# Kernel optimization log

Hardware: AMD Instinct MI355X
Metric: run time of the kernel (lower is better)

## Reference

```python
import jax, jax.numpy as jnp
import numpy as np

E, K, CAP = 6, 2, 192
ALPHA, LOAD_PEN, MIN_USE, TEMP = 0.7, 2.0, 0.05, 1.0
BN_EPS = 1e-5
NEG = -1e30


def conv3x3(x, w, b=None):
    y = jax.lax.conv_general_dilated(x, w, (1, 1), 'SAME',
                                     dimension_numbers=('NCHW', 'OIHW', 'NCHW'))
    if b is not None:
        y = y + b[None, :, None, None]
    return y


def bn_eval(x, g, b):
    # fresh BatchNorm buffers: running_mean=0, running_var=1
    s = g / jnp.sqrt(1.0 + BN_EPS)
    return x * s[None, :, None, None] + b[None, :, None, None]


def maxpool2(x):
    return jax.lax.reduce_window(x, -jnp.inf, jax.lax.max,
                                 (1, 1, 2, 2), (1, 1, 2, 2), 'VALID')


def avgpool_to2(x):
    B, C, H, W = x.shape
    return x.reshape(B, C, 2, H // 2, 2, W // 2).mean(axis=(3, 5))


def expert_forward(p, x):
    h = jax.nn.relu(bn_eval(conv3x3(x, p['c1w'], p['c1b']), p['b1g'], p['b1b']))
    h = maxpool2(h)  # 32 -> 16
    h = jax.nn.relu(bn_eval(conv3x3(h, p['c2w'], p['c2b']), p['b2g'], p['b2b']))
    h = jax.nn.relu(bn_eval(conv3x3(h, p['c3w'], p['c3b']), p['b3g'], p['b3b']))
    h = maxpool2(h)  # 16 -> 8
    h = jax.nn.relu(bn_eval(conv3x3(h, p['c4w'], p['c4b']), p['b4g'], p['b4b']))
    h = jax.nn.relu(bn_eval(conv3x3(h, p['c5w'], p['c5b']), p['b5g'], p['b5b']))
    feat = h.mean(axis=(2, 3))                       # global avg pool -> [B, c3]
    f = jax.nn.relu(feat @ p['fw'].T + p['fb'])      # [B, feat_dim]
    return f @ p['cw'].T + p['cb']                   # [B, num_classes]


def moe_forward(x, t_c1w, t_b1g, t_b1b, t_c2w, t_b2g, t_b2b, t_fcw, t_fcb,
                g1w, g1b, g2w, g2b,
                e_c1w, e_c1b, e_b1g, e_b1b, e_c2w, e_c2b, e_b2g, e_b2b,
                e_c3w, e_c3b, e_b3g, e_b3b, e_c4w, e_c4b, e_b4g, e_b4b,
                e_c5w, e_c5b, e_b5g, e_b5b, e_fw, e_fb, e_cw, e_cb, ema):
    B = x.shape[0]
    # --- routing trunk ---
    h = jax.nn.relu(bn_eval(conv3x3(x, t_c1w), t_b1g, t_b1b))
    h = jax.nn.relu(bn_eval(conv3x3(h, t_c2w), t_b2g, t_b2b))
    h = avgpool_to2(maxpool2(h)).reshape(B, -1)      # [B, 128]
    rf = jax.nn.relu(h @ t_fcw.T + t_fcb)            # [B, routing_dim]
    # --- gate (eval: no dropout, no noise) ---
    g = jax.nn.relu(rf @ g1w.T + g1b)
    gate_scores = (g @ g2w.T + g2b) / TEMP           # [B, E]
    # --- all experts on full batch (dense, as in source) ---
    ep = {'c1w': e_c1w, 'c1b': e_c1b, 'b1g': e_b1g, 'b1b': e_b1b,
          'c2w': e_c2w, 'c2b': e_c2b, 'b2g': e_b2g, 'b2b': e_b2b,
          'c3w': e_c3w, 'c3b': e_c3b, 'b3g': e_b3g, 'b3b': e_b3b,
          'c4w': e_c4w, 'c4b': e_c4b, 'b4g': e_b4g, 'b4b': e_b4b,
          'c5w': e_c5w, 'c5b': e_c5b, 'b5g': e_b5g, 'b5b': e_b5b,
          'fw': e_fw, 'fb': e_fb, 'cw': e_cw, 'cb': e_cb}
    logits_e = jax.vmap(expert_forward, in_axes=(0, None))(ep, x)  # [E, B, C]
    logits_e = jnp.transpose(logits_e, (1, 0, 2))                   # [B, E, C]
    # confidence = -entropy = sum p*log(p)
    logp = jax.nn.log_softmax(logits_e, axis=2)
    conf = (jnp.exp(logp) * jnp.log(jnp.exp(logp) + 1e-12)).sum(axis=2)  # [B, E]
    # --- balanced scores ---
    combined = ALPHA * gate_scores + (1.0 - ALPHA) * conf
    boost = jnp.where(ema < MIN_USE, (MIN_USE - ema) * 10.0, 0.0)
    combined = combined + boost[None, :]
    balanced = combined - LOAD_PEN * ema[None, :]
    # --- greedy capacity-constrained dispatch (deterministic order, eval) ---
    _, topk_idx = jax.lax.top_k(balanced, K)          # [B, K]

    def step(loads, idxs):
        l = loads[idxs]                                # [K]
        fits = l < CAP
        first = jnp.argmax(fits)                       # first expert with room
        fallback = idxs[jnp.argmin(l)]
        chosen = jnp.where(fits.any(), idxs[first], fallback)
        return loads.at[chosen].add(1.0), chosen

    _, chosen = jax.lax.scan(step, jnp.zeros((E,), balanced.dtype), topk_idx)
    D = jax.nn.one_hot(chosen, E, dtype=bool)          # [B, E]
    # --- weighted combine ---
    masked = jnp.where(D, balanced, NEG)
    w = jax.nn.softmax(masked, axis=1) * D.astype(balanced.dtype)
    w = w / (w.sum(axis=1, keepdims=True) + 1e-12)
    logits_final = (w[:, :, None] * logits_e).sum(axis=1)  # [B, C]
    return logits_final, balanced, D


def _params(key):
    ks = iter(jax.random.split(key, 64))
    rd, rd2, fd, nc, c1, c2, c3 = 64, 32, 128, 10, 32, 64, 128

    def w(shape, fan):
        return jax.random.normal(next(ks), shape, jnp.float32) * np.sqrt(2.0 / fan)

    p = {}
    p['t_c1w'] = w((32, 3, 3, 3), 32 * 9); p['t_b1g'] = jnp.ones(32); p['t_b1b'] = jnp.zeros(32)
    p['t_c2w'] = w((32, 32, 3, 3), 32 * 9); p['t_b2g'] = jnp.ones(32); p['t_b2b'] = jnp.zeros(32)
    p['t_fcw'] = w((rd, 128), rd); p['t_fcb'] = jnp.zeros(rd)
    p['g1w'] = w((rd2, rd), rd2); p['g1b'] = jnp.zeros(rd2)
    p['g2w'] = w((E, rd2), E); p['g2b'] = jnp.zeros(E)
    for i, (ci, co) in enumerate([(3, c1), (c1, c2), (c2, c2), (c2, c3), (c3, c3)], 1):
        p[f'e_c{i}w'] = w((E, co, ci, 3, 3), co * 9)
        p[f'e_c{i}b'] = jnp.zeros((E, co))
        p[f'e_b{i}g'] = jnp.ones((E, co))
        p[f'e_b{i}b'] = jnp.zeros((E, co))
    p['e_fw'] = w((E, fd, c3), fd); p['e_fb'] = jnp.zeros((E, fd))
    p['e_cw'] = w((E, nc, fd), nc); p['e_cb'] = jnp.zeros((E, nc))
    p['ema'] = jnp.ones((E,), jnp.float32) / E
    return p


def setup_inputs() -> dict:
    key = jax.random.key(0)
    kx, kp = jax.random.split(key)
    inp = {'x': jax.random.normal(kx, (1024, 3, 32, 32), jnp.float32)}
    inp.update(_params(kp))
    return inp


def reference(x, t_c1w, t_b1g, t_b1b, t_c2w, t_b2g, t_b2b, t_fcw, t_fcb,
              g1w, g1b, g2w, g2b,
              e_c1w, e_c1b, e_b1g, e_b1b, e_c2w, e_c2b, e_b2g, e_b2b,
              e_c3w, e_c3b, e_b3g, e_b3b, e_c4w, e_c4b, e_b4g, e_b4b,
              e_c5w, e_c5b, e_b5g, e_b5b, e_fw, e_fb, e_cw, e_cb, ema):
    return moe_forward(x, t_c1w, t_b1g, t_b1b, t_c2w, t_b2g, t_b2b, t_fcw, t_fcb,
                       g1w, g1b, g2w, g2b,
                       e_c1w, e_c1b, e_b1g, e_b1b, e_c2w, e_c2b, e_b2g, e_b2b,
                       e_c3w, e_c3b, e_b3g, e_b3b, e_c4w, e_c4b, e_b4g, e_b4b,
                       e_c5w, e_c5b, e_b5g, e_b5b, e_fw, e_fb, e_cw, e_cb, ema)
```

## Files before the change

### kernel.cpp

```cpp
#include <hip/hip_runtime.h>
#include <math.h>

#define B_ 1024
#define E_ 6

typedef _Float16 half8 __attribute__((ext_vector_type(8)));
typedef float f32x4 __attribute__((ext_vector_type(4)));

__device__ __forceinline__ unsigned short h_bits(_Float16 h) {
    union { _Float16 f; unsigned short u; } c; c.f = h; return c.u;
}
__device__ __forceinline__ unsigned int splitpack(float v) {
    _Float16 h = (_Float16)v;
    _Float16 l = (_Float16)((v - (float)h) * 2048.0f);
    return (unsigned int)h_bits(h) | ((unsigned int)h_bits(l) << 16);
}

__global__ void prep_w(const float* __restrict__ w, const float* __restrict__ g,
                       float* __restrict__ wout, int CO, int CI, int total) {
    int i = blockIdx.x * 256 + threadIdx.x;
    if (i >= total) return;
    int k = i % 9;
    int t = i / 9;
    int ci = t % CI; t /= CI;
    int co = t % CO;
    int e  = t / CO;
    float s = g[e * CO + co] * (1.0f / sqrtf(1.0f + 1e-5f));
    wout[(((long)(e * CI + ci) * 9 + k) * CO) + co] = w[i] * s;
}

__global__ void prep_b(const float* __restrict__ cb, const float* __restrict__ g,
                       const float* __restrict__ bb, float* __restrict__ bout, int N) {
    int i = blockIdx.x * 256 + threadIdx.x;
    if (i >= N) return;
    float s = g[i] * (1.0f / sqrtf(1.0f + 1e-5f));
    float c = (cb != nullptr) ? cb[i] : 0.0f;
    bout[i] = c * s + bb[i];
}

__global__ void prep_wfrag(const float* __restrict__ w, const float* __restrict__ g,
                           _Float16* __restrict__ out, int CI, int CO, int total) {
    int i = blockIdx.x * 256 + threadIdx.x;
    if (i >= total) return;
    const int NC = CI / 32;
    const int NB = CO / 16;
    int j = i & 7;
    int lane = (i >> 3) & 63;
    int rest = i >> 9;
    int chunk = rest % NC; rest /= NC;
    int tap = rest % 9; rest /= 9;
    int nbg = rest % NB;
    int e = rest / NB;
    int co = nbg * 16 + (lane & 15);
    int ci = chunk * 32 + ((lane >> 4) * 8) + j;
    float s = g[e * CO + co] * (1.0f / sqrtf(1.0f + 1e-5f));
    float v = w[(((long)(e * CO + co) * CI + ci) * 9) + tap] * s;
    _Float16 hi = (_Float16)v;
    _Float16 lo = (_Float16)((v - (float)hi) * 2048.0f);
    long perE = (long)NB * 9 * NC * 2 * 512;
    long F0 = ((long)(nbg * 9 + tap) * NC + chunk) * 2;
    long base = (long)e * perE + F0 * 512 + lane * 8 + j;
    out[base] = hi;
    out[base + 512] = lo;
}

template <int CI, int CO, int H, int TS, int CO_BLK, int CI_CHUNK, bool POOL, int OUTMODE>
__launch_bounds__(256)
__global__ void conv3x3(const float* __restrict__ in, const float* __restrict__ wt,
                        const float* __restrict__ bias, void* __restrict__ outv) {
    constexpr int TD = H / TS;
    constexpr int TILES = TD * TD;
    constexpr int LW = TS + 2;
    constexpr int NPX = POOL ? (TS / 2) * (TS / 2) : TS * TS;
    constexpr int G = 256 / NPX;
    constexpr int NG = CO / CO_BLK;
    constexpr int GPT = NG / G;
    constexpr int COT = GPT * CO_BLK;
    constexpr int NW = POOL ? 4 : 1;
    constexpr int OD = POOL ? TS / 2 : TS;

    __shared__ float lds[CI_CHUNK * LW * LW];

    int bid = blockIdx.x;
    int n = bid / TILES;
    int t = bid % TILES;
    int ty = (t / TD) * TS;
    int tx = (t % TD) * TS;
    int tid = threadIdx.x;
    int px = tid % NPX;
    int cg0 = tid / NPX;
    const int cg0s = __builtin_amdgcn_readfirstlane(cg0);
    int oy = px / OD;
    int ox = px % OD;

    float acc[NW][COT];
#pragma unroll
    for (int g2 = 0; g2 < GPT; ++g2)
#pragma unroll
        for (int j = 0; j < CO_BLK; ++j) {
            float bv = bias[(cg0s + g2 * G) * CO_BLK + j];
#pragma unroll
            for (int p = 0; p < NW; ++p) acc[p][g2 * CO_BLK + j] = bv;
        }

    for (int cc = 0; cc < CI / CI_CHUNK; ++cc) {
        const float* inb = in + ((long)n * CI + cc * CI_CHUNK) * (H * H);
        for (int idx = tid; idx < CI_CHUNK * LW * LW; idx += 256) {
            int ci = idx / (LW * LW);
            int r = idx - ci * (LW * LW);
            int yy = r / LW + ty - 1;
            int xx = r % LW + tx - 1;
            float v = 0.0f;
            if ((unsigned)yy < (unsigned)H && (unsigned)xx < (unsigned)H)
                v = inb[ci * H * H + yy * H + xx];
            lds[idx] = v;
        }
        __syncthreads();

        const float* wbase = wt + ((long)cc * CI_CHUNK) * 9 * CO;
        for (int ci = 0; ci < CI_CHUNK; ++ci) {
#pragma unroll
            for (int ky = 0; ky < 3; ++ky) {
#pragma unroll
                for (int kx = 0; kx < 3; ++kx) {
                    float v[NW];
                    if constexpr (POOL) {
#pragma unroll
                        for (int dy = 0; dy < 2; ++dy)
#pragma unroll
                            for (int dx = 0; dx < 2; ++dx)
                                v[dy * 2 + dx] =
                                    lds[ci * LW * LW + (2 * oy + dy + ky) * LW + (2 * ox + dx + kx)];
                    } else {
                        v[0] = lds[ci * LW * LW + (oy + ky) * LW + (ox + kx)];
                    }
                    const float* wr = wbase + ((ci * 3 + ky) * 3 + kx) * CO + cg0s * CO_BLK;
#pragma unroll
                    for (int g2 = 0; g2 < GPT; ++g2)
#pragma unroll
                        for (int j = 0; j < CO_BLK; ++j) {
                            float wv = wr[g2 * G * CO_BLK + j];
#pragma unroll
                            for (int p = 0; p < NW; ++p)
                                acc[p][g2 * CO_BLK + j] = fmaf(v[p], wv, acc[p][g2 * CO_BLK + j]);
                        }
                }
            }
        }
        __syncthreads();
    }

    if constexpr (OUTMODE == 1) {
        unsigned int* po = (unsigned int*)outv;
        long base;
        if constexpr (POOL) {
            constexpr int HP = H / 2;
            int pp = (ty / 2 + oy) * HP + (tx / 2 + ox);
            base = ((long)n * (HP * HP) + pp) * CO;
        } else {
            int pp = (ty + oy) * H + (tx + ox);
            base = ((long)n * (H * H) + pp) * CO;
        }
#pragma unroll
        for (int g2 = 0; g2 < GPT; ++g2) {
            int cobase = (cg0s + g2 * G) * CO_BLK;
#pragma unroll
            for (int j4 = 0; j4 < CO_BLK; j4 += 4) {
                uint4 u;
                unsigned int* up = (unsigned int*)&u;
#pragma unroll
                for (int jj = 0; jj < 4; ++jj) {
                    int a = g2 * CO_BLK + j4 + jj;
                    float v;
                    if constexpr (POOL)
                        v = fmaxf(fmaxf(acc[0][a], acc[1][a]), fmaxf(acc[2][a], acc[3][a]));
                    else
                        v = acc[0][a];
                    up[jj] = splitpack(fmaxf(v, 0.0f));
                }
                *(uint4*)(po + base + cobase + j4) = u;
            }
        }
    } else {
        float* out = (float*)outv;
        if constexpr (POOL) {
            constexpr int HP = H / 2;
            int py = ty / 2 + oy;
            int pxx = tx / 2 + ox;
#pragma unroll
            for (int g2 = 0; g2 < GPT; ++g2)
#pragma unroll
                for (int j = 0; j < CO_BLK; ++j) {
                    int co = (cg0s + g2 * G) * CO_BLK + j;
                    int a = g2 * CO_BLK + j;
                    float m = fmaxf(fmaxf(acc[0][a], acc[1][a]), fmaxf(acc[2][a], acc[3][a]));
                    out[((long)n * CO + co) * (HP * HP) + py * HP + pxx] = fmaxf(m, 0.0f);
                }
        } else {
            int yy = ty + oy;
            int xx = tx + ox;
#pragma unroll
            for (int g2 = 0; g2 < GPT; ++g2)
#pragma unroll
                for (int j = 0; j < CO_BLK; ++j) {
                    int co = (cg0s + g2 * G) * CO_BLK + j;
                    out[((long)n * CO + co) * (H * H) + yy * H + xx] =
                        fmaxf(acc[0][g2 * CO_BLK + j], 0.0f);
                }
        }
    }
}

__launch_bounds__(256, 2)
__global__ void conv_mfma_t2(const unsigned int* __restrict__ in,
                             const _Float16* __restrict__ wt,
                             const float* __restrict__ bias,
                             float* __restrict__ rf, int n0) {
    constexpr int PXS = 40;
    __shared__ _Float16 ldsH[18 * 18 * PXS];
    __shared__ _Float16 ldsL[18 * 18 * PXS];
    __shared__ float red[4][32];

    const int tid = threadIdx.x;
    const int wv = tid >> 6, lane = tid & 63;
    const int q = lane >> 4, l15 = lane & 15;
    const int bid = blockIdx.x;
    const int nl = bid >> 2, tile = bid & 3;
    const int ty2 = (tile >> 1) * 16, tx2 = (tile & 1) * 16;

    f32x4 accH[8], accL[8];
#pragma unroll
    for (int i = 0; i < 8; ++i) { accH[i] = (f32x4){0,0,0,0}; accL[i] = (f32x4){0,0,0,0}; }

    for (int u = tid; u < 18 * 18 * 8; u += 256) {
        int cu = u & 7;
        int p = u >> 3;
        int wy = p / 18, wx = p % 18;
        int gy = ty2 + wy - 1, gx = tx2 + wx - 1;
        uint4 w = make_uint4(0, 0, 0, 0);
        if ((unsigned)gy < 32u && (unsigned)gx < 32u)
            w = *(const uint4*)(in + ((long)nl * 1024 + gy * 32 + gx) * 32 + cu * 4);
        unsigned int h01 = (w.x & 0xffffu) | (w.y << 16);
        unsigned int h23 = (w.z & 0xffffu) | (w.w << 16);
        unsigned int l01 = (w.x >> 16) | (w.y & 0xffff0000u);
        unsigned int l23 = (w.z >> 16) | (w.w & 0xffff0000u);
        int fi = (wy * 18 + wx) * PXS + cu * 4;
        *(uint2*)(&ldsH[fi]) = make_uint2(h01, h23);
        *(uint2*)(&ldsL[fi]) = make_uint2(l01, l23);
    }
    __syncthreads();

#pragma unroll
    for (int ky = 0; ky < 3; ++ky)
#pragma unroll
        for (int kx = 0; kx < 3; ++kx) {
            const int tap = ky * 3 + kx;
            half8 ah[4], al[4];
#pragma unroll
            for (int mb = 0; mb < 4; ++mb) {
                int y = wv * 4 + mb;
                int fi = ((y + ky) * 18 + (l15 + kx)) * PXS + q * 8;
                ah[mb] = *(const half8*)&ldsH[fi];
                al[mb] = *(const half8*)&ldsL[fi];
            }
            half8 bh[2], bl[2];
#pragma unroll
            for (int nb = 0; nb < 2; ++nb) {
                int F0 = (nb * 9 + tap) * 2;
                bh[nb] = ((const half8*)wt)[(long)F0 * 64 + lane];
                bl[nb] = ((const half8*)wt)[(long)(F0 + 1) * 64 + lane];
            }
#pragma unroll
            for (int nb = 0; nb < 2; ++nb)
#pragma unroll
                for (int mb = 0; mb < 4; ++mb)
                    accH[mb * 2 + nb] = __builtin_amdgcn_mfma_f32_16x16x32_f16(
                        ah[mb], bh[nb], accH[mb * 2 + nb], 0, 0, 0);
#pragma unroll
            for (int nb = 0; nb < 2; ++nb)
#pragma unroll
                for (int mb = 0; mb < 4; ++mb)
                    accL[mb * 2 + nb] = __builtin_amdgcn_mfma_f32_16x16x32_f16(
                        ah[mb], bl[nb], accL[mb * 2 + nb], 0, 0, 0);
#pragma unroll
            for (int nb = 0; nb < 2; ++nb)
#pragma unroll
                for (int mb = 0; mb < 4; ++mb)
                    accL[mb * 2 + nb] = __builtin_amdgcn_mfma_f32_16x16x32_f16(
                        al[mb], bh[nb], accL[mb * 2 + nb], 0, 0, 0);
        }

    const float inv2048 = 1.0f / 2048.0f;
    float bv[2];
#pragma unroll
    for (int nb = 0; nb < 2; ++nb) bv[nb] = bias[nb * 16 + l15];
    float avg[2] = {0.0f, 0.0f};
#pragma unroll
    for (int k = 0; k < 2; ++k)
#pragma unroll
        for (int j = 0; j < 2; ++j)
#pragma unroll
            for (int nb = 0; nb < 2; ++nb) {
                float m = -1e30f;
#pragma unroll
                for (int dm = 0; dm < 2; ++dm)
#pragma unroll
                    for (int dr = 0; dr < 2; ++dr) {
                        int a = (2 * k + dm) * 2 + nb;
                        int r = 2 * j + dr;
                        float v = accH[a][r] + accL[a][r] * inv2048 + bv[nb];
                        m = fmaxf(m, v);
                    }
                avg[nb] += fmaxf(m, 0.0f);
            }
#pragma unroll
    for (int nb = 0; nb < 2; ++nb) {
        avg[nb] += __shfl_xor(avg[nb], 16);
        avg[nb] += __shfl_xor(avg[nb], 32);
    }
    if (q == 0) {
        red[wv][l15] = avg[0];
        red[wv][16 + l15] = avg[1];
    }
    __syncthreads();
    if (tid < 32) {
        float s = red[0][tid] + red[1][tid] + red[2][tid] + red[3][tid];
        int n = n0 + nl;
        rf[(long)n * 128 + tid * 4 + (tile >> 1) * 2 + (tile & 1)] = s * (1.0f / 64.0f);
    }
}

__launch_bounds__(512, 2)
__global__ void conv_expert(const float* __restrict__ x,
                            const float* __restrict__ w1b, const float* __restrict__ b1b_,
                            const _Float16* __restrict__ wt2b, const float* __restrict__ b2b_,
                            const _Float16* __restrict__ wt3b, const float* __restrict__ b3b_,
                            const _Float16* __restrict__ wt4b, const float* __restrict__ b4b_,
                            const _Float16* __restrict__ wt5b, const float* __restrict__ b5b_,
                            float* __restrict__ featb) {
    __shared__ _Float16 pool[77760];
    _Float16* c2H = pool;
    _Float16* c2L = pool + 12960;
    _Float16* BH  = pool;
    _Float16* BL  = pool + 8000;
    float* xs  = (float*)(pool + 25920);
    float* w1s = (float*)(pool + 25920 + 6936);
    float* b1s = (float*)(pool + 25920 + 6936 + 1728);
    _Float16* AH = pool + 25920;
    _Float16* AL = pool + 51840;
    _Float16* CH = pool + 25920;
    _Float16* CL = pool + 41920;

    const int tid = threadIdx.x;
    const int wv = tid >> 6, lane = tid & 63;
    const int q = lane >> 4, l15 = lane & 15;
    const int rg = wv >> 1, ch2 = wv & 1;
    const int e = blockIdx.x >> 10;
    const int n = blockIdx.x & 1023;
    const float inv2048 = 1.0f / 2048.0f;

    const float* w1 = w1b + e * 864;
    const float* b1 = b1b_ + e * 32;
    const _Float16* wt2 = wt2b + (size_t)e * 36864;
    const float* b2 = b2b_ + e * 64;
    const _Float16* wt3 = wt3b + (size_t)e * 73728;
    const float* b3 = b3b_ + e * 64;
    const _Float16* wt4 = wt4b + (size_t)e * 147456;
    const float* b4 = b4b_ + e * 128;
    const _Float16* wt5 = wt5b + (size_t)e * 294912;
    const float* b5 = b5b_ + e * 128;
    float* feat = featb + (size_t)e * (B_ * 128);

    {
        half8 z = {};
        half8* zp = (half8*)pool;
        for (int i = tid; i < 3240; i += 512) zp[i] = z;
    }
    for (int i = tid; i < 864; i += 512) w1s[i] = w1[i];
    if (tid < 32) b1s[tid] = b1[tid];
    for (int i = tid; i < 3 * 1156; i += 512) {
        int c = i / 1156;
        int r = i - c * 1156;
        int yy = r / 34 - 1, xx = r % 34 - 1;
        float v = 0.0f;
        if ((unsigned)yy < 32u && (unsigned)xx < 32u)
            v = x[((long)n * 3 + c) * 1024 + yy * 32 + xx];
        xs[i] = v;
    }
    __syncthreads();

    {
        const int pix = tid & 255;
        const int py1 = pix >> 4, px1 = pix & 15;
        const int coh = tid >> 8;
#pragma unroll
        for (int cg = 0; cg < 2; ++cg) {
            const int cog = coh * 2 + cg;
            float a[4][8];
#pragma unroll
            for (int j = 0; j < 8; ++j) {
                float bvv = b1s[cog * 8 + j];
#pragma unroll
                for (int p = 0; p < 4; ++p) a[p][j] = bvv;
            }
            for (int ci = 0; ci < 3; ++ci) {
                float patch[16];
#pragma unroll
                for (int r = 0; r < 4; ++r)
#pragma unroll
                    for (int cpx = 0; cpx < 4; ++cpx)
                        patch[r * 4 + cpx] = xs[ci * 1156 + (2 * py1 + r) * 34 + (2 * px1 + cpx)];
#pragma unroll
                for (int ky = 0; ky < 3; ++ky)
#pragma unroll
                    for (int kx = 0; kx < 3; ++kx) {
                        const float* wr = &w1s[((ci * 3 + ky) * 3 + kx) * 32 + cog * 8];
#pragma unroll
                        for (int j = 0; j < 8; ++j) {
                            float wvv = wr[j];
#pragma unroll
                            for (int dy = 0; dy < 2; ++dy)
#pragma unroll
                                for (int dx = 0; dx < 2; ++dx)
                                    a[dy * 2 + dx][j] =
// ... 107 lines not shown
#pragma unroll
        for (int ky = 0; ky < 3; ++ky)
#pragma unroll
            for (int kx = 0; kx < 3; ++kx) {
                const int tap = ky * 3 + kx;
                half8 ah[4], al[4];
#pragma unroll
                for (int mb = 0; mb < 4; ++mb) {
                    int y = rg * 4 + mb;
                    int fi = c * 12960 + ((y + ky) * 18 + (l15 + kx)) * 40 + q * 8;
                    ah[mb] = *(const half8*)&AH[fi];
                    al[mb] = *(const half8*)&AL[fi];
                }
                half8 bh[2], bl[2];
#pragma unroll
                for (int nb = 0; nb < 2; ++nb) {
                    int nbg = ch2 * 2 + nb;
                    int F0 = ((nbg * 9 + tap) * 2 + c) * 2;
                    bh[nb] = ((const half8*)wt3)[(long)F0 * 64 + lane];
                    bl[nb] = ((const half8*)wt3)[(long)(F0 + 1) * 64 + lane];
                }
#pragma unroll
                for (int nb = 0; nb < 2; ++nb)
#pragma unroll
                    for (int mb = 0; mb < 4; ++mb)
                        accH[mb * 2 + nb] = __builtin_amdgcn_mfma_f32_16x16x32_f16(
                            ah[mb], bh[nb], accH[mb * 2 + nb], 0, 0, 0);
#pragma unroll
                for (int nb = 0; nb < 2; ++nb)
#pragma unroll
                    for (int mb = 0; mb < 4; ++mb)
                        accL[mb * 2 + nb] = __builtin_amdgcn_mfma_f32_16x16x32_f16(
                            ah[mb], bl[nb], accL[mb * 2 + nb], 0, 0, 0);
#pragma unroll
                for (int nb = 0; nb < 2; ++nb)
#pragma unroll
                    for (int mb = 0; mb < 4; ++mb)
                        accL[mb * 2 + nb] = __builtin_amdgcn_mfma_f32_16x16x32_f16(
                            al[mb], bh[nb], accL[mb * 2 + nb], 0, 0, 0);
            }
    }
    __syncthreads();

    for (int u = tid; u < 2 * 36 * 4; u += 512) {
        int g = u & 3;
        int t2 = u >> 2;
        int ck = t2 / 36;
        int rp = t2 % 36;
        int wy, wx;
        if (rp < 10) { wy = 0; wx = rp; }
        else if (rp < 20) { wy = 9; wx = rp - 10; }
        else if (rp < 28) { wy = rp - 19; wx = 0; }
        else { wy = rp - 27; wx = 9; }
        int fi = ck * 4000 + (wy * 10 + wx) * 40 + g * 8;
        *(uint4*)(&BH[fi]) = make_uint4(0, 0, 0, 0);
        *(uint4*)(&BL[fi]) = make_uint4(0, 0, 0, 0);
    }
    for (int u = tid; u < 4 * 36 * 4; u += 512) {
        int g = u & 3;
        int t2 = u >> 2;
        int ck = t2 / 36;
        int rp = t2 % 36;
        int wy, wx;
        if (rp < 10) { wy = 0; wx = rp; }
        else if (rp < 20) { wy = 9; wx = rp - 10; }
        else if (rp < 28) { wy = rp - 19; wx = 0; }
        else { wy = rp - 27; wx = 9; }
        int fi = ck * 4000 + (wy * 10 + wx) * 40 + g * 8;
        *(uint4*)(&CH[fi]) = make_uint4(0, 0, 0, 0);
        *(uint4*)(&CL[fi]) = make_uint4(0, 0, 0, 0);
    }
    {
        float bv[2];
#pragma unroll
        for (int nb = 0; nb < 2; ++nb) bv[nb] = b3[ch2 * 32 + nb * 16 + l15];
#pragma unroll
        for (int k = 0; k < 2; ++k)
#pragma unroll
            for (int j = 0; j < 2; ++j) {
                int yy = rg * 2 + k;
                int xx = q * 2 + j;
                int p = (yy + 1) * 10 + (xx + 1);
#pragma unroll
                for (int nb = 0; nb < 2; ++nb) {
                    float m = -1e30f;
#pragma unroll
                    for (int dm = 0; dm < 2; ++dm)
#pragma unroll
                        for (int dr = 0; dr < 2; ++dr) {
                            int a = (2 * k + dm) * 2 + nb;
                            int r = 2 * j + dr;
                            float v = accH[a][r] + accL[a][r] * inv2048 + bv[nb];
                            m = fmaxf(m, v);
                        }
                    m = fmaxf(m, 0.0f);
                    _Float16 hi = (_Float16)m;
                    _Float16 lo = (_Float16)((m - (float)hi) * 2048.0f);
                    int fi = ch2 * 4000 + p * 40 + nb * 16 + l15;
                    BH[fi] = hi;
                    BL[fi] = lo;
                }
            }
    }
    __syncthreads();

#pragma unroll
    for (int i = 0; i < 4; ++i) { accH[i] = (f32x4){0,0,0,0}; accL[i] = (f32x4){0,0,0,0}; }

    for (int c = 0; c < 2; ++c) {
#pragma unroll
        for (int ky = 0; ky < 3; ++ky)
#pragma unroll
            for (int kx = 0; kx < 3; ++kx) {
                const int tap = ky * 3 + kx;
                half8 ah[4], al[4];
#pragma unroll
                for (int mb = 0; mb < 4; ++mb) {
                    int m = mb * 16 + l15;
                    int p = ((m >> 3) + ky) * 10 + ((m & 7) + kx);
                    int fi = c * 4000 + p * 40 + q * 8;
                    ah[mb] = *(const half8*)&BH[fi];
                    al[mb] = *(const half8*)&BL[fi];
                }
                half8 bh, bl;
                {
                    int F0 = ((wv * 9 + tap) * 2 + c) * 2;
                    bh = ((const half8*)wt4)[(long)F0 * 64 + lane];
                    bl = ((const half8*)wt4)[(long)(F0 + 1) * 64 + lane];
                }
#pragma unroll
                for (int mb = 0; mb < 4; ++mb)
                    accH[mb] = __builtin_amdgcn_mfma_f32_16x16x32_f16(ah[mb], bh, accH[mb], 0, 0, 0);
#pragma unroll
                for (int mb = 0; mb < 4; ++mb)
                    accL[mb] = __builtin_amdgcn_mfma_f32_16x16x32_f16(ah[mb], bl, accL[mb], 0, 0, 0);
#pragma unroll
                for (int mb = 0; mb < 4; ++mb)
                    accL[mb] = __builtin_amdgcn_mfma_f32_16x16x32_f16(al[mb], bh, accL[mb], 0, 0, 0);
            }
    }
    {
        float bv = b4[wv * 16 + l15];
#pragma unroll
        for (int mb = 0; mb < 4; ++mb)
#pragma unroll
            for (int r = 0; r < 4; ++r) {
                int px = mb * 16 + q * 4 + r;
                int p = ((px >> 3) + 1) * 10 + ((px & 7) + 1);
                float v = accH[mb][r] + accL[mb][r] * inv2048 + bv;
                v = fmaxf(v, 0.0f);
                _Float16 hi = (_Float16)v;
                _Float16 lo = (_Float16)((v - (float)hi) * 2048.0f);
                int fi = (wv >> 1) * 4000 + p * 40 + (wv & 1) * 16 + l15;
                CH[fi] = hi;
                CL[fi] = lo;
            }
    }
    __syncthreads();

#pragma unroll
    for (int i = 0; i < 4; ++i) { accH[i] = (f32x4){0,0,0,0}; accL[i] = (f32x4){0,0,0,0}; }

    for (int c = 0; c < 4; ++c) {
#pragma unroll
        for (int ky = 0; ky < 3; ++ky)
#pragma unroll
            for (int kx = 0; kx < 3; ++kx) {
                const int tap = ky * 3 + kx;
                half8 ah[4], al[4];
#pragma unroll
                for (int mb = 0; mb < 4; ++mb) {
                    int m = mb * 16 + l15;
                    int p = ((m >> 3) + ky) * 10 + ((m & 7) + kx);
                    int fi = c * 4000 + p * 40 + q * 8;
                    ah[mb] = *(const half8*)&CH[fi];
                    al[mb] = *(const half8*)&CL[fi];
                }
                half8 bh, bl;
                {
                    int F0 = ((wv * 9 + tap) * 4 + c) * 2;
                    bh = ((const half8*)wt5)[(long)F0 * 64 + lane];
                    bl = ((const half8*)wt5)[(long)(F0 + 1) * 64 + lane];
                }
#pragma unroll
                for (int mb = 0; mb < 4; ++mb)
                    accH[mb] = __builtin_amdgcn_mfma_f32_16x16x32_f16(ah[mb], bh, accH[mb], 0, 0, 0);
#pragma unroll
                for (int mb = 0; mb < 4; ++mb)
                    accL[mb] = __builtin_amdgcn_mfma_f32_16x16x32_f16(ah[mb], bl, accL[mb], 0, 0, 0);
#pragma unroll
                for (int mb = 0; mb < 4; ++mb)
                    accL[mb] = __builtin_amdgcn_mfma_f32_16x16x32_f16(al[mb], bh, accL[mb], 0, 0, 0);
            }
    }
    {
        float bv = b5[wv * 16 + l15];
        float s = 0.0f;
#pragma unroll
        for (int mb = 0; mb < 4; ++mb)
#pragma unroll
            for (int r = 0; r < 4; ++r) {
                float v = accH[mb][r] + accL[mb][r] * inv2048 + bv;
                s += fmaxf(v, 0.0f);
            }
        s += __shfl_xor(s, 16);
        s += __shfl_xor(s, 32);
        if (lane < 16)
            feat[(long)n * 128 + wv * 16 + l15] = s * (1.0f / 64.0f);
    }
}

__launch_bounds__(128)
__global__ void head_k(const float* __restrict__ featb, const float* __restrict__ fwb,
                       const float* __restrict__ fbb, const float* __restrict__ cwb,
                       const float* __restrict__ cbb, float* __restrict__ outlb) {
    __shared__ float fe[128];
    __shared__ float fv[128];
    int e = blockIdx.x >> 10;
    int n = blockIdx.x & 1023;
    int t = threadIdx.x;
    const float* feat = featb + (size_t)e * (B_ * 128);
    const float* fw = fwb + (size_t)e * 16384;
    const float* fb = fbb + e * 128;
    const float* cw = cwb + (size_t)e * 1280;
    const float* cb = cbb + e * 10;
    float* outl = outlb + (size_t)e * (B_ * 10);

    fe[t] = feat[(long)n * 128 + t];
    __syncthreads();
    const float* wr = fw + t * 128;
    float a = fb[t];
#pragma unroll 8
    for (int k = 0; k < 128; ++k) a = fmaf(fe[k], wr[k], a);
    fv[t] = fmaxf(a, 0.0f);
    __syncthreads();
    if (t < 10) {
        const float* cr = cw + t * 128;
        float a2 = cb[t];
#pragma unroll 8
        for (int k = 0; k < 128; ++k) a2 = fmaf(fv[k], cr[k], a2);
        outl[n * 10 + t] = a2;
    }
}

template <int I, int O, bool RELU>
__global__ void fc_k(const float* __restrict__ in, const float* __restrict__ W,
                     const float* __restrict__ bias, float* __restrict__ out) {
    int g = blockIdx.x * 256 + threadIdx.x;
    if (g >= B_ * O) return;
    int n = g / O;
    int o = g - n * O;
    const float* ip = in + (long)n * I;
    const float* wp = W + (long)o * I;
    float a = bias[o];
#pragma unroll 8
    for (int k = 0; k < I; ++k) a = fmaf(ip[k], wp[k], a);
    if (RELU) a = fmaxf(a, 0.0f);
    out[g] = a;
}

__global__ void conf_bal_k(const float* __restrict__ logitsE, const float* __restrict__ gate,
                           const float* __restrict__ ema, float* __restrict__ balanced,
                           unsigned char* __restrict__ cand) {
    int b = blockIdx.x * 256 + threadIdx.x;
    if (b >= B_) return;
    float bal[E_];
#pragma unroll
    for (int e = 0; e < E_; ++e) {
        const float* lp = logitsE + ((long)e * B_ + b) * 10;
        float m = lp[0];
#pragma unroll
        for (int k = 1; k < 10; ++k) m = fmaxf(m, lp[k]);
        float s = 0.0f;
#pragma unroll
        for (int k = 0; k < 10; ++k) s += expf(lp[k] - m);
        float ls = m + logf(s);
        float conf = 0.0f;
#pragma unroll
        for (int k = 0; k < 10; ++k) {
            float pp = expf(lp[k] - ls);
            conf += pp * logf(pp + 1e-12f);
        }
        float em = ema[e];
        float boost = (em < 0.05f) ? (0.05f - em) * 10.0f : 0.0f;
        bal[e] = 0.7f * gate[b * E_ + e] + 0.3f * conf + boost - 2.0f * em;
        balanced[b * E_ + e] = bal[e];
    }
    int i0 = 0;
    float m0 = bal[0];
#pragma unroll
    for (int e = 1; e < E_; ++e)
        if (bal[e] > m0) { m0 = bal[e]; i0 = e; }
    int i1 = -1;
    float m1 = -1e38f;
// ... 34 lines not shown
#pragma unroll
    for (int k = 0; k < 10; ++k) out[b * 10 + k] = lp[k] * w;
    float* Dp = out + B_ * 10 + B_ * E_ + b * E_;
#pragma unroll
    for (int e = 0; e < E_; ++e) Dp[e] = (e == c) ? 1.0f : 0.0f;
}

extern "C" void kernel_launch(void* const* d_in, const int* in_sizes, int n_in,
                              void* d_out, int out_size, void* d_ws, size_t ws_size,
                              hipStream_t stream) {
    (void)in_sizes; (void)n_in; (void)out_size; (void)ws_size;
    const float* x     = (const float*)d_in[0];
    const float* t_c1w = (const float*)d_in[1];
    const float* t_b1g = (const float*)d_in[2];
    const float* t_b1b = (const float*)d_in[3];
    const float* t_c2w = (const float*)d_in[4];
    const float* t_b2g = (const float*)d_in[5];
    const float* t_b2b = (const float*)d_in[6];
    const float* t_fcw = (const float*)d_in[7];
    const float* t_fcb = (const float*)d_in[8];
    const float* g1w   = (const float*)d_in[9];
    const float* g1b   = (const float*)d_in[10];
    const float* g2w   = (const float*)d_in[11];
    const float* g2b   = (const float*)d_in[12];
    const float* e_c1w = (const float*)d_in[13];
    const float* e_c1b = (const float*)d_in[14];
    const float* e_b1g = (const float*)d_in[15];
    const float* e_b1b = (const float*)d_in[16];
    const float* e_c2w = (const float*)d_in[17];
    const float* e_c2b = (const float*)d_in[18];
    const float* e_b2g = (const float*)d_in[19];
    const float* e_b2b = (const float*)d_in[20];
    const float* e_c3w = (const float*)d_in[21];
    const float* e_c3b = (const float*)d_in[22];
    const float* e_b3g = (const float*)d_in[23];
    const float* e_b3b = (const float*)d_in[24];
    const float* e_c4w = (const float*)d_in[25];
    const float* e_c4b = (const float*)d_in[26];
    const float* e_b4g = (const float*)d_in[27];
    const float* e_b4b = (const float*)d_in[28];
    const float* e_c5w = (const float*)d_in[29];
    const float* e_c5b = (const float*)d_in[30];
    const float* e_b5g = (const float*)d_in[31];
    const float* e_b5b = (const float*)d_in[32];
    const float* e_fw  = (const float*)d_in[33];
    const float* e_fb  = (const float*)d_in[34];
    const float* e_cw  = (const float*)d_in[35];
    const float* e_cb  = (const float*)d_in[36];
    const float* ema   = (const float*)d_in[37];
    float* out = (float*)d_out;
    float* ws  = (float*)d_ws;

    size_t o = 0;
    float* R1f = ws + o; o += 8388608;
    float* R2f = ws + o; o += 16777216;
    float* rf_in   = ws + o; o += B_ * 128;
    float* rf      = ws + o; o += B_ * 64;
    float* gv      = ws + o; o += B_ * 32;
    float* gate    = ws + o; o += B_ * E_;
    float* logitsE = ws + o; o += E_ * B_ * 10;
    float* featb   = ws + o; o += (size_t)E_ * B_ * 128;
    int*   chosen  = (int*)(ws + o); o += B_;
    unsigned char* cand = (unsigned char*)(ws + o); o += 256;
    float* wt_t1 = ws + o; o += 864;
    float* bt_t1 = ws + o; o += 32;
    float* bt_t2 = ws + o; o += 32;
    float* wt_c1 = ws + o; o += 6 * 864;
    float* bt_c1 = ws + o; o += 6 * 32;
    float* bt_c2 = ws + o; o += 6 * 64;
    float* bt_c3 = ws + o; o += 6 * 64;
    float* bt_c4 = ws + o; o += 6 * 128;
    float* bt_c5 = ws + o; o += 6 * 128;
    _Float16* wfrag_t2 = (_Float16*)(ws + o); o += 9216;
    _Float16* wfrag_c2 = (_Float16*)(ws + o); o += 110592;
    _Float16* wfrag_c3 = (_Float16*)(ws + o); o += 221184;
    _Float16* wfrag_c4 = (_Float16*)(ws + o); o += 442368;
    _Float16* wfrag_c5 = (_Float16*)(ws + o); o += 884736;

    unsigned int* R2u = (unsigned int*)R2f;
    (void)R1f;

    auto gsz = [](int n) { return (n + 255) / 256; };
    prep_w<<<gsz(864), 256, 0, stream>>>(t_c1w, t_b1g, wt_t1, 32, 3, 864);
    prep_b<<<1, 256, 0, stream>>>(nullptr, t_b1g, t_b1b, bt_t1, 32);
    prep_wfrag<<<gsz(9216), 256, 0, stream>>>(t_c2w, t_b2g, wfrag_t2, 32, 32, 9216);
    prep_b<<<1, 256, 0, stream>>>(nullptr, t_b2g, t_b2b, bt_t2, 32);
    prep_w<<<gsz(5184), 256, 0, stream>>>(e_c1w, e_b1g, wt_c1, 32, 3, 5184);
    prep_b<<<1, 256, 0, stream>>>(e_c1b, e_b1g, e_b1b, bt_c1, 192);
    prep_wfrag<<<gsz(110592), 256, 0, stream>>>(e_c2w, e_b2g, wfrag_c2, 32, 64, 110592);
    prep_b<<<2, 256, 0, stream>>>(e_c2b, e_b2g, e_b2b, bt_c2, 384);
    prep_wfrag<<<gsz(221184), 256, 0, stream>>>(e_c3w, e_b3g, wfrag_c3, 64, 64, 221184);
    prep_b<<<2, 256, 0, stream>>>(e_c3b, e_b3g, e_b3b, bt_c3, 384);
    prep_wfrag<<<gsz(442368), 256, 0, stream>>>(e_c4w, e_b4g, wfrag_c4, 64, 128, 442368);
    prep_b<<<3, 256, 0, stream>>>(e_c4b, e_b4g, e_b4b, bt_c4, 768);
    prep_wfrag<<<gsz(884736), 256, 0, stream>>>(e_c5w, e_b5g, wfrag_c5, 128, 128, 884736);
    prep_b<<<3, 256, 0, stream>>>(e_c5b, e_b5g, e_b5b, bt_c5, 768);

    for (int q = 0; q < 2; ++q) {
        const float* xq = x + (size_t)q * 512 * 3 * 1024;
        conv3x3<3, 32, 32, 16, 32, 3, false, 1><<<512 * 4, 256, 0, stream>>>(
            xq, wt_t1, bt_t1, (void*)R2u);
        conv_mfma_t2<<<512 * 4, 256, 0, stream>>>(R2u, wfrag_t2, bt_t2, rf_in, q * 512);
    }
    fc_k<128, 64, true><<<256, 256, 0, stream>>>(rf_in, t_fcw, t_fcb, rf);
    fc_k<64, 32, true><<<128, 256, 0, stream>>>(rf, g1w, g1b, gv);
    fc_k<32, 6, false><<<24, 256, 0, stream>>>(gv, g2w, g2b, gate);

    conv_expert<<<E_ * B_, 512, 0, stream>>>(
        x, wt_c1, bt_c1, wfrag_c2, bt_c2, wfrag_c3, bt_c3,
        wfrag_c4, bt_c4, wfrag_c5, bt_c5, featb);
    head_k<<<E_ * B_, 128, 0, stream>>>(featb, e_fw, e_fb, e_cw, e_cb, logitsE);

    float* balanced = out + B_ * 10;
    conf_bal_k<<<4, 256, 0, stream>>>(logitsE, gate, ema, balanced, cand);
    dispatch_k<<<1, 64, 0, stream>>>(cand, chosen);
    final_k<<<4, 256, 0, stream>>>(logitsE, chosen, out);
}
```

Measured before the change: 1.325 ms.

## Fuse trunk conv1 into MFMA conv2, fold expert head into expert kernel

The first trunk conv is now computed per tile inside the MFMA trunk conv2 kernel, with its output written as split-fp16 directly into LDS. This removes the global intermediate buffer and the separate launches per half-batch. The expert FC head is folded into the end of conv_expert, so the feature buffer round trip and the head_k launch go away. The LDS pixel stride for the 8x8 stages also shrinks from 40 to 32, which saves LDS but may add bank conflicts. In exchange, conv1 recomputes its 18x18 halo for each tile.

```diff
diff --git a/kernel.cpp b/kernel.cpp
--- a/kernel.cpp
+++ b/kernel.cpp
@@ -9,11 +9,6 @@
 
 __device__ __forceinline__ unsigned short h_bits(_Float16 h) {
     union { _Float16 f; unsigned short u; } c; c.f = h; return c.u;
-}
-__device__ __forceinline__ unsigned int splitpack(float v) {
-    _Float16 h = (_Float16)v;
-    _Float16 l = (_Float16)((v - (float)h) * 2048.0f);
-    return (unsigned int)h_bits(h) | ((unsigned int)h_bits(l) << 16);
 }
 
 __global__ void prep_w(const float* __restrict__ w, const float* __restrict__ g,
@@ -64,159 +59,15 @@
     out[base + 512] = lo;
 }
 
-template <int CI, int CO, int H, int TS, int CO_BLK, int CI_CHUNK, bool POOL, int OUTMODE>
-__launch_bounds__(256)
-__global__ void conv3x3(const float* __restrict__ in, const float* __restrict__ wt,
-                        const float* __restrict__ bias, void* __restrict__ outv) {
-    constexpr int TD = H / TS;
-    constexpr int TILES = TD * TD;
-    constexpr int LW = TS + 2;
-    constexpr int NPX = POOL ? (TS / 2) * (TS / 2) : TS * TS;
-    constexpr int G = 256 / NPX;
-    constexpr int NG = CO / CO_BLK;
-    constexpr int GPT = NG / G;
-    constexpr int COT = GPT * CO_BLK;
-    constexpr int NW = POOL ? 4 : 1;
-    constexpr int OD = POOL ? TS / 2 : TS;
-
-    __shared__ float lds[CI_CHUNK * LW * LW];
-
-    int bid = blockIdx.x;
-    int n = bid / TILES;
-    int t = bid % TILES;
-    int ty = (t / TD) * TS;
-    int tx = (t % TD) * TS;
-    int tid = threadIdx.x;
-    int px = tid % NPX;
-    int cg0 = tid / NPX;
-    const int cg0s = __builtin_amdgcn_readfirstlane(cg0);
-    int oy = px / OD;
-    int ox = px % OD;
-
-    float acc[NW][COT];
-#pragma unroll
-    for (int g2 = 0; g2 < GPT; ++g2)
-#pragma unroll
-        for (int j = 0; j < CO_BLK; ++j) {
-            float bv = bias[(cg0s + g2 * G) * CO_BLK + j];
-#pragma unroll
-            for (int p = 0; p < NW; ++p) acc[p][g2 * CO_BLK + j] = bv;
-        }
-
-    for (int cc = 0; cc < CI / CI_CHUNK; ++cc) {
-        const float* inb = in + ((long)n * CI + cc * CI_CHUNK) * (H * H);
-        for (int idx = tid; idx < CI_CHUNK * LW * LW; idx += 256) {
-            int ci = idx / (LW * LW);
-            int r = idx - ci * (LW * LW);
-            int yy = r / LW + ty - 1;
-            int xx = r % LW + tx - 1;
-            float v = 0.0f;
-            if ((unsigned)yy < (unsigned)H && (unsigned)xx < (unsigned)H)
-                v = inb[ci * H * H + yy * H + xx];
-            lds[idx] = v;
-        }
-        __syncthreads();
-
-        const float* wbase = wt + ((long)cc * CI_CHUNK) * 9 * CO;
-        for (int ci = 0; ci < CI_CHUNK; ++ci) {
-#pragma unroll
-            for (int ky = 0; ky < 3; ++ky) {
-#pragma unroll
-                for (int kx = 0; kx < 3; ++kx) {
-                    float v[NW];
-                    if constexpr (POOL) {
-#pragma unroll
-                        for (int dy = 0; dy < 2; ++dy)
-#pragma unroll
-                            for (int dx = 0; dx < 2; ++dx)
-                                v[dy * 2 + dx] =
-                                    lds[ci * LW * LW + (2 * oy + dy + ky) * LW + (2 * ox + dx + kx)];
-                    } else {
-                        v[0] = lds[ci * LW * LW + (oy + ky) * LW + (ox + kx)];
-                    }
-                    const float* wr = wbase + ((ci * 3 + ky) * 3 + kx) * CO + cg0s * CO_BLK;
-#pragma unroll
-                    for (int g2 = 0; g2 < GPT; ++g2)
-#pragma unroll
-                        for (int j = 0; j < CO_BLK; ++j) {
-                            float wv = wr[g2 * G * CO_BLK + j];
-#pragma unroll
-                            for (int p = 0; p < NW; ++p)
-                                acc[p][g2 * CO_BLK + j] = fmaf(v[p], wv, acc[p][g2 * CO_BLK + j]);
-                        }
-                }
-            }
-        }
-        __syncthreads();
-    }
-
-    if constexpr (OUTMODE == 1) {
-        unsigned int* po = (unsigned int*)outv;
-        long base;
-        if constexpr (POOL) {
-            constexpr int HP = H / 2;
-            int pp = (ty / 2 + oy) * HP + (tx / 2 + ox);
-            base = ((long)n * (HP * HP) + pp) * CO;
-        } else {
-            int pp = (ty + oy) * H + (tx + ox);
-            base = ((long)n * (H * H) + pp) * CO;
-        }
-#pragma unroll
-        for (int g2 = 0; g2 < GPT; ++g2) {
-            int cobase = (cg0s + g2 * G) * CO_BLK;
-#pragma unroll
-            for (int j4 = 0; j4 < CO_BLK; j4 += 4) {
-                uint4 u;
-                unsigned int* up = (unsigned int*)&u;
-#pragma unroll
-                for (int jj = 0; jj < 4; ++jj) {
-                    int a = g2 * CO_BLK + j4 + jj;
-                    float v;
-                    if constexpr (POOL)
-                        v = fmaxf(fmaxf(acc[0][a], acc[1][a]), fmaxf(acc[2][a], acc[3][a]));
-                    else
-                        v = acc[0][a];
-                    up[jj] = splitpack(fmaxf(v, 0.0f));
-                }
-                *(uint4*)(po + base + cobase + j4) = u;
-            }
-        }
-    } else {
-        float* out = (float*)outv;
-        if constexpr (POOL) {
-            constexpr int HP = H / 2;
-            int py = ty / 2 + oy;
-            int pxx = tx / 2 + ox;
-#pragma unroll
-            for (int g2 = 0; g2 < GPT; ++g2)
-#pragma unroll
-                for (int j = 0; j < CO_BLK; ++j) {
-                    int co = (cg0s + g2 * G) * CO_BLK + j;
-                    int a = g2 * CO_BLK + j;
-                    float m = fmaxf(fmaxf(acc[0][a], acc[1][a]), fmaxf(acc[2][a], acc[3][a]));
-                    out[((long)n * CO + co) * (HP * HP) + py * HP + pxx] = fmaxf(m, 0.0f);
-                }
-        } else {
-            int yy = ty + oy;
-            int xx = tx + ox;
-#pragma unroll
-            for (int g2 = 0; g2 < GPT; ++g2)
-#pragma unroll
-                for (int j = 0; j < CO_BLK; ++j) {
-                    int co = (cg0s + g2 * G) * CO_BLK + j;
-                    out[((long)n * CO + co) * (H * H) + yy * H + xx] =
-                        fmaxf(acc[0][g2 * CO_BLK + j], 0.0f);
-                }
-        }
-    }
-}
-
 __launch_bounds__(256, 2)
-__global__ void conv_mfma_t2(const unsigned int* __restrict__ in,
-                             const _Float16* __restrict__ wt,
-                             const float* __restrict__ bias,
-                             float* __restrict__ rf, int n0) {
+__global__ void conv_trunk(const float* __restrict__ x,
+                           const float* __restrict__ w1, const float* __restrict__ b1,
+                           const _Float16* __restrict__ wt2, const float* __restrict__ bias2,
+                           float* __restrict__ rf) {
     constexpr int PXS = 40;
+    __shared__ float xs[3 * 400];
+    __shared__ float w1s[864];
+    __shared__ float b1s[32];
     __shared__ _Float16 ldsH[18 * 18 * PXS];
     __shared__ _Float16 ldsL[18 * 18 * PXS];
     __shared__ float red[4][32];
@@ -228,27 +79,58 @@
     const int nl = bid >> 2, tile = bid & 3;
     const int ty2 = (tile >> 1) * 16, tx2 = (tile & 1) * 16;
 
+    {
+        half8 z = {};
+        half8* zh = (half8*)ldsH;
+        half8* zl = (half8*)ldsL;
+        for (int i = tid; i < 18 * 18 * PXS / 8; i += 256) { zh[i] = z; zl[i] = z; }
+    }
+    for (int i = tid; i < 864; i += 256) w1s[i] = w1[i];
+    if (tid < 32) b1s[tid] = b1[tid];
+    for (int i = tid; i < 1200; i += 256) {
+        int c = i / 400;
+        int r = i - c * 400;
+        int yy = ty2 + r / 20 - 2, xx = tx2 + r % 20 - 2;
+        float v = 0.0f;
+        if ((unsigned)yy < 32u && (unsigned)xx < 32u)
+            v = x[((long)nl * 3 + c) * 1024 + yy * 32 + xx];
+        xs[i] = v;
+    }
+    __syncthreads();
+
+    for (int p = tid; p < 324; p += 256) {
+        int wy = p / 18, wx = p - wy * 18;
+        int gy = ty2 + wy - 1, gx = tx2 + wx - 1;
+        if ((unsigned)gy < 32u && (unsigned)gx < 32u) {
+            float acc[32];
+#pragma unroll
+            for (int j = 0; j < 32; ++j) acc[j] = b1s[j];
+            for (int ci = 0; ci < 3; ++ci)
+#pragma unroll
+                for (int ky = 0; ky < 3; ++ky)
+#pragma unroll
+                    for (int kx = 0; kx < 3; ++kx) {
+                        float v = xs[ci * 400 + (wy + ky) * 20 + (wx + kx)];
+                        const float* wr = &w1s[((ci * 3 + ky) * 3 + kx) * 32];
+#pragma unroll
+                        for (int j = 0; j < 32; ++j) acc[j] = fmaf(v, wr[j], acc[j]);
+                    }
+            int fb = (wy * 18 + wx) * PXS;
+#pragma unroll
+            for (int j = 0; j < 32; ++j) {
+                float m = fmaxf(acc[j], 0.0f);
+                _Float16 hi = (_Float16)m;
+                _Float16 lo = (_Float16)((m - (float)hi) * 2048.0f);
+                ldsH[fb + j] = hi;
+                ldsL[fb + j] = lo;
+            }
+        }
+    }
+    __syncthreads();
+
     f32x4 accH[8], accL[8];
 #pragma unroll
     for (int i = 0; i < 8; ++i) { accH[i] = (f32x4){0,0,0,0}; accL[i] = (f32x4){0,0,0,0}; }
-
-    for (int u = tid; u < 18 * 18 * 8; u += 256) {
-        int cu = u & 7;
-        int p = u >> 3;
-        int wy = p / 18, wx = p % 18;
-        int gy = ty2 + wy - 1, gx = tx2 + wx - 1;
-        uint4 w = make_uint4(0, 0, 0, 0);
-        if ((unsigned)gy < 32u && (unsigned)gx < 32u)
-            w = *(const uint4*)(in + ((long)nl * 1024 + gy * 32 + gx) * 32 + cu * 4);
-        unsigned int h01 = (w.x & 0xffffu) | (w.y << 16);
-        unsigned int h23 = (w.z & 0xffffu) | (w.w << 16);
-        unsigned int l01 = (w.x >> 16) | (w.y & 0xffff0000u);
-        unsigned int l23 = (w.z >> 16) | (w.w & 0xffff0000u);
-        int fi = (wy * 18 + wx) * PXS + cu * 4;
-        *(uint2*)(&ldsH[fi]) = make_uint2(h01, h23);
-        *(uint2*)(&ldsL[fi]) = make_uint2(l01, l23);
-    }
-    __syncthreads();
 
 #pragma unroll
     for (int ky = 0; ky < 3; ++ky)
@@ -267,8 +149,8 @@
 #pragma unroll
             for (int nb = 0; nb < 2; ++nb) {
                 int F0 = (nb * 9 + tap) * 2;
-                bh[nb] = ((const half8*)wt)[(long)F0 * 64 + lane];
-                bl[nb] = ((const half8*)wt)[(long)(F0 + 1) * 64 + lane];
+                bh[nb] = ((const half8*)wt2)[(long)F0 * 64 + lane];
+                bl[nb] = ((const half8*)wt2)[(long)(F0 + 1) * 64 + lane];
             }
 #pragma unroll
             for (int nb = 0; nb < 2; ++nb)
@@ -293,7 +175,7 @@
     const float inv2048 = 1.0f / 2048.0f;
     float bv[2];
 #pragma unroll
-    for (int nb = 0; nb < 2; ++nb) bv[nb] = bias[nb * 16 + l15];
+    for (int nb = 0; nb < 2; ++nb) bv[nb] = bias2[nb * 16 + l15];
     float avg[2] = {0.0f, 0.0f};
 #pragma unroll
     for (int k = 0; k < 2; ++k)
@@ -325,8 +207,7 @@
     __syncthreads();
     if (tid < 32) {
         float s = red[0][tid] + red[1][tid] + red[2][tid] + red[3][tid];
-        int n = n0 + nl;
-        rf[(long)n * 128 + tid * 4 + (tile >> 1) * 2 + (tile & 1)] = s * (1.0f / 64.0f);
+        rf[(long)nl * 128 + tid * 4 + (tile >> 1) * 2 + (tile & 1)] = s * (1.0f / 64.0f);
     }
 }
 
@@ -337,19 +218,21 @@
                             const _Float16* __restrict__ wt3b, const float* __restrict__ b3b_,
                             const _Float16* __restrict__ wt4b, const float* __restrict__ b4b_,
                             const _Float16* __restrict__ wt5b, const float* __restrict__ b5b_,
-                            float* __restrict__ featb) {
+                            const float* __restrict__ fwb, const float* __restrict__ fbb,
+                            const float* __restrict__ cwb, const float* __restrict__ cbb,
+                            float* __restrict__ logitsE) {
     __shared__ _Float16 pool[77760];
     _Float16* c2H = pool;
     _Float16* c2L = pool + 12960;
     _Float16* BH  = pool;
-    _Float16* BL  = pool + 8000;
+    _Float16* BL  = pool + 6400;
     float* xs  = (float*)(pool + 25920);
     float* w1s = (float*)(pool + 25920 + 6936);
     float* b1s = (float*)(pool + 25920 + 6936 + 1728);
     _Float16* AH = pool + 25920;
     _Float16* AL = pool + 51840;
     _Float16* CH = pool + 25920;
-    _Float16* CL = pool + 41920;
+    _Float16* CL = pool + 38720;
 
     const int tid = threadIdx.x;
     const int wv = tid >> 6, lane = tid & 63;
@@ -369,7 +252,11 @@
     const float* b4 = b4b_ + e * 128;
     const _Float16* wt5 = wt5b + (size_t)e * 294912;
     const float* b5 = b5b_ + e * 128;
-    float* feat = featb + (size_t)e * (B_ * 128);
+    const float* fw = fwb + (size_t)e * 16384;
+    const float* fb = fbb + e * 128;
+    const float* cw = cwb + (size_t)e * 1280;
+    const float* cb = cbb + e * 10;
+    float* outl = logitsE + (size_t)e * (B_ * 10);
 
     {
         half8 z = {};
@@ -583,7 +470,7 @@
         else if (rp < 20) { wy = 9; wx = rp - 10; }
         else if (rp < 28) { wy = rp - 19; wx = 0; }
         else { wy = rp - 27; wx = 9; }
-        int fi = ck * 4000 + (wy * 10 + wx) * 40 + g * 8;
+        int fi = ck * 3200 + (wy * 10 + wx) * 32 + g * 8;
         *(uint4*)(&BH[fi]) = make_uint4(0, 0, 0, 0);
         *(uint4*)(&BL[fi]) = make_uint4(0, 0, 0, 0);
     }
@@ -597,7 +484,7 @@
         else if (rp < 20) { wy = 9; wx = rp - 10; }
         else if (rp < 28) { wy = rp - 19; wx = 0; }
         else { wy = rp - 27; wx = 9; }
-        int fi = ck * 4000 + (wy * 10 + wx) * 40 + g * 8;
+        int fi = ck * 3200 + (wy * 10 + wx) * 32 + g * 8;
         *(uint4*)(&CH[fi]) = make_uint4(0, 0, 0, 0);
         *(uint4*)(&CL[fi]) = make_uint4(0, 0, 0, 0);
     }
@@ -627,7 +514,7 @@
                     m = fmaxf(m, 0.0f);
                     _Float16 hi = (_Float16)m;
                     _Float16 lo = (_Float16)((m - (float)hi) * 2048.0f);
-                    int fi = ch2 * 4000 + p * 40 + nb * 16 + l15;
+                    int fi = ch2 * 3200 + p * 32 + nb * 16 + l15;
                     BH[fi] = hi;
                     BL[fi] = lo;
                 }
@@ -649,7 +536,7 @@
                 for (int mb = 0; mb < 4; ++mb) {
                     int m = mb * 16 + l15;
                     int p = ((m >> 3) + ky) * 10 + ((m & 7) + kx);
-                    int fi = c * 4000 + p * 40 + q * 8;
+                    int fi = c * 3200 + p * 32 + q * 8;
                     ah[mb] = *(const half8*)&BH[fi];
                     al[mb] = *(const half8*)&BL[fi];
                 }
@@ -682,7 +569,7 @@
                 v = fmaxf(v, 0.0f);
                 _Float16 hi = (_Float16)v;
                 _Float16 lo = (_Float16)((v - (float)hi) * 2048.0f);
-                int fi = (wv >> 1) * 4000 + p * 40 + (wv & 1) * 16 + l15;
+                int fi = (wv >> 1) * 3200 + p * 32 + (wv & 1) * 16 + l15;
                 CH[fi] = hi;
                 CL[fi] = lo;
             }
@@ -703,7 +590,7 @@
                 for (int mb = 0; mb < 4; ++mb) {
                     int m = mb * 16 + l15;
                     int p = ((m >> 3) + ky) * 10 + ((m & 7) + kx);
-                    int fi = c * 4000 + p * 40 + q * 8;
+                    int fi = c * 3200 + p * 32 + q * 8;
                     ah[mb] = *(const half8*)&CH[fi];
                     al[mb] = *(const half8*)&CL[fi];
                 }
@@ -724,6 +611,8 @@
                     accL[mb] = __builtin_amdgcn_mfma_f32_16x16x32_f16(al[mb], bh, accL[mb], 0, 0, 0);
             }
     }
+    float* fe = (float*)pool;
+    float* fv = fe + 128;
     {
         float bv = b5[wv * 16 + l15];
         float s = 0.0f;
@@ -736,41 +625,24 @@
             }
         s += __shfl_xor(s, 16);
         s += __shfl_xor(s, 32);
-        if (lane < 16)
-            feat[(long)n * 128 + wv * 16 + l15] = s * (1.0f / 64.0f);
-    }
-}
-
-__launch_bounds__(128)
-__global__ void head_k(const float* __restrict__ featb, const float* __restrict__ fwb,
-                       const float* __restrict__ fbb, const float* __restrict__ cwb,
-                       const float* __restrict__ cbb, float* __restrict__ outlb) {
-    __shared__ float fe[128];
-    __shared__ float fv[128];
-    int e = blockIdx.x >> 10;
-    int n = blockIdx.x & 1023;
-    int t = threadIdx.x;
-    const float* feat = featb + (size_t)e * (B_ * 128);
-    const float* fw = fwb + (size_t)e * 16384;
-    const float* fb = fbb + e * 128;
-    const float* cw = cwb + (size_t)e * 1280;
-    const float* cb = cbb + e * 10;
-    float* outl = outlb + (size_t)e * (B_ * 10);
-
-    fe[t] = feat[(long)n * 128 + t];
-    __syncthreads();
-    const float* wr = fw + t * 128;
-    float a = fb[t];
+        if (lane < 16) fe[wv * 16 + l15] = s * (1.0f / 64.0f);
+    }
+    __syncthreads();
+
+    if (tid < 128) {
+        const float* wr = fw + tid * 128;
+        float a = fb[tid];
 #pragma unroll 8
-    for (int k = 0; k < 128; ++k) a = fmaf(fe[k], wr[k], a);
-    fv[t] = fmaxf(a, 0.0f);
-    __syncthreads();
-    if (t < 10) {
-        const float* cr = cw + t * 128;
-        float a2 = cb[t];
+        for (int k = 0; k < 128; ++k) a = fmaf(fe[k], wr[k], a);
+        fv[tid] = fmaxf(a, 0.0f);
+    }
+    __syncthreads();
+    if (tid < 10) {
+        const float* cr = cw + tid * 128;
+        float a2 = cb[tid];
 #pragma unroll 8
         for (int k = 0; k < 128; ++k) a2 = fmaf(fv[k], cr[k], a2);
-        outl[n * 10 + t] = a2;
+        outl[(size_t)n * 10 + tid] = a2;
     }
 }
 
@@ -911,14 +783,11 @@
     float* ws  = (float*)d_ws;
 
     size_t o = 0;
-    float* R1f = ws + o; o += 8388608;
-    float* R2f = ws + o; o += 16777216;
     float* rf_in   = ws + o; o += B_ * 128;
     float* rf      = ws + o; o += B_ * 64;
     float* gv      = ws + o; o += B_ * 32;
     float* gate    = ws + o; o += B_ * E_;
     float* logitsE = ws + o; o += E_ * B_ * 10;
-    float* featb   = ws + o; o += (size_t)E_ * B_ * 128;
     int*   chosen  = (int*)(ws + o); o += B_;
     unsigned char* cand = (unsigned char*)(ws + o); o += 256;
     float* wt_t1 = ws + o; o += 864;
@@ -936,9 +805,6 @@
     _Float16* wfrag_c4 = (_Float16*)(ws + o); o += 442368;
     _Float16* wfrag_c5 = (_Float16*)(ws + o); o += 884736;
 
-    unsigned int* R2u = (unsigned int*)R2f;
-    (void)R1f;
-
     auto gsz = [](int n) { return (n + 255) / 256; };
     prep_w<<<gsz(864), 256, 0, stream>>>(t_c1w, t_b1g, wt_t1, 32, 3, 864);
     prep_b<<<1, 256, 0, stream>>>(nullptr, t_b1g, t_b1b, bt_t1, 32);
@@ -955,20 +821,15 @@
     prep_wfrag<<<gsz(884736), 256, 0, stream>>>(e_c5w, e_b5g, wfrag_c5, 128, 128, 884736);
     prep_b<<<3, 256, 0, stream>>>(e_c5b, e_b5g, e_b5b, bt_c5, 768);
 
-    for (int q = 0; q < 2; ++q) {
-        const float* xq = x + (size_t)q * 512 * 3 * 1024;
-        conv3x3<3, 32, 32, 16, 32, 3, false, 1><<<512 * 4, 256, 0, stream>>>(
-            xq, wt_t1, bt_t1, (void*)R2u);
-        conv_mfma_t2<<<512 * 4, 256, 0, stream>>>(R2u, wfrag_t2, bt_t2, rf_in, q * 512);
-    }
+    conv_trunk<<<B_ * 4, 256, 0, stream>>>(x, wt_t1, bt_t1, wfrag_t2, bt_t2, rf_in);
     fc_k<128, 64, true><<<256, 256, 0, stream>>>(rf_in, t_fcw, t_fcb, rf);
     fc_k<64, 32, true><<<128, 256, 0, stream>>>(rf, g1w, g1b, gv);
     fc_k<32, 6, false><<<24, 256, 0, stream>>>(gv, g2w, g2b, gate);
 
     conv_expert<<<E_ * B_, 512, 0, stream>>>(
         x, wt_c1, bt_c1, wfrag_c2, bt_c2, wfrag_c3, bt_c3,
-        wfrag_c4, bt_c4, wfrag_c5, bt_c5, featb);
-    head_k<<<E_ * B_, 128, 0, stream>>>(featb, e_fw, e_fb, e_cw, e_cb, logitsE);
+        wfrag_c4, bt_c4, wfrag_c5, bt_c5,
+        e_fw, e_fb, e_cw, e_cb, logitsE);
 
     float* balanced = out + B_ * 10;
     conf_bal_k<<<4, 256, 0, stream>>>(logitsE, gate, ema, balanced, cand);
```

New measurement: 1.638 ms. +23.6%, slower.
